# Optimization experiments

Measured on AMD Instinct MI355X. Metric: run time of the kernel, lower is better.

Reference implementation:

```python
import jax, jax.numpy as jnp
import numpy as np

B, T, D = 32, 2048, 512

def setup_inputs() -> dict:
    key = jax.random.key(0)
    k1, k2, k3 = jax.random.split(key, 3)
    return {
        "query": jax.random.normal(k1, (B, D), dtype=jnp.float32),
        "key": jax.random.normal(k2, (B, T, D), dtype=jnp.float32),
        "value": jax.random.normal(k3, (B, T, D), dtype=jnp.float32),
    }

def reference(query, key, value):
    # energy: [B, T] = bmm(key [B,T,D], query [B,D,1]).squeeze
    energy = jnp.einsum("btd,bd->bt", key, query)
    attention = jax.nn.softmax(energy, axis=1)  # over T, no scaling/masking (faithful)
    # context: [B, D] = bmm(attention [B,1,T], value [B,T,D]).squeeze
    out = jnp.einsum("bt,btd->bd", attention, value)
    return (out, attention)
```

## Files before the change

kernel.cpp:

```cpp
#include <hip/hip_runtime.h>

#define B_ 32
#define T_ 2048
#define D_ 512

__global__ __launch_bounds__(256) void energy_stats_kernel(
    const float* __restrict__ q,
    const float* __restrict__ key,
    float* __restrict__ energy,
    float* __restrict__ stats,
    float* __restrict__ out)
{
    const int b    = blockIdx.x >> 6;
    const int sub  = blockIdx.x & 63;
    const int wave = threadIdx.x >> 6;
    const int lane = threadIdx.x & 63;

    if (sub == 0 && threadIdx.x < 128) {
        const float4 z = {0.f, 0.f, 0.f, 0.f};
        ((float4*)out)[b * 128 + threadIdx.x] = z;
    }

    __shared__ float es[32];

    const float4 qv0 = ((const float4*)q)[b * 128 + lane];
    const float4 qv1 = ((const float4*)q)[b * 128 + 64 + lane];

    const int t0 = sub * 32 + wave * 8;
    const float4* kbase = (const float4*)key + ((size_t)b * T_ + t0) * 128;

#pragma unroll
    for (int r = 0; r < 8; ++r) {
        const float4 k0 = kbase[r * 128 + lane];
        const float4 k1 = kbase[r * 128 + 64 + lane];
        float acc = k0.x * qv0.x + k0.y * qv0.y + k0.z * qv0.z + k0.w * qv0.w
                  + k1.x * qv1.x + k1.y * qv1.y + k1.z * qv1.z + k1.w * qv1.w;
#pragma unroll
        for (int off = 32; off >= 1; off >>= 1)
            acc += __shfl_down(acc, off);
        if (lane == 0) {
            es[wave * 8 + r] = acc;
            energy[b * T_ + t0 + r] = acc;
        }
    }
    __syncthreads();

    if (threadIdx.x < 32) {
        const float e = es[threadIdx.x];
        float m = e;
#pragma unroll
        for (int off = 16; off >= 1; off >>= 1)
            m = fmaxf(m, __shfl_xor(m, off));
        float s = __expf(e - m);
#pragma unroll
        for (int off = 16; off >= 1; off >>= 1)
            s += __shfl_xor(s, off);
        if (threadIdx.x == 0) {
            stats[((size_t)b * 64 + sub) * 2 + 0] = m;
            stats[((size_t)b * 64 + sub) * 2 + 1] = s;
        }
    }
}

__global__ __launch_bounds__(256) void context_kernel(
    const float* __restrict__ energy,
    const float* __restrict__ stats,
    const float* __restrict__ value,
    float* __restrict__ attn,
    float* __restrict__ out)
{
    const int b   = blockIdx.x >> 6;
    const int sub = blockIdx.x & 63;
    const int t0  = sub * 32;
    const int tid = threadIdx.x;

    __shared__ float  MS[2];
    __shared__ float  attn_s[32];
    __shared__ float4 red4[128];

    if (tid < 64) {
        const float m_c = stats[((size_t)b * 64 + tid) * 2 + 0];
        const float s_c = stats[((size_t)b * 64 + tid) * 2 + 1];
        float M = m_c;
#pragma unroll
        for (int off = 32; off >= 1; off >>= 1)
            M = fmaxf(M, __shfl_xor(M, off));
        float S = s_c * __expf(m_c - M);
#pragma unroll
        for (int off = 32; off >= 1; off >>= 1)
            S += __shfl_xor(S, off);
        if (tid == 0) { MS[0] = M; MS[1] = S; }
    }
    __syncthreads();
    const float M    = MS[0];
    const float invS = 1.f / MS[1];

    if (tid < 32) {
        const float e = energy[b * T_ + t0 + tid];
        const float a = __expf(e - M) * invS;
        attn_s[tid] = a;
        attn[b * T_ + t0 + tid] = a;
    }
    __syncthreads();

    const int tg = tid >> 7;
    const int d4 = tid & 127;

    const float4* v4 = (const float4*)value + ((size_t)b * T_ + t0 + tg) * 128 + d4;
    float4 acc = {0.f, 0.f, 0.f, 0.f};
#pragma unroll
    for (int i = 0; i < 16; ++i) {
        const float a = attn_s[2 * i + tg];
        const float4 vv = v4[i * 256];
        acc.x += a * vv.x; acc.y += a * vv.y;
        acc.z += a * vv.z; acc.w += a * vv.w;
    }

    if (tg == 1) red4[d4] = acc;
    __syncthreads();
    if (tg == 0) {
        const float4 o = red4[d4];
        acc.x += o.x; acc.y += o.y; acc.z += o.z; acc.w += o.w;
        float* dst = out + (size_t)b * D_ + d4 * 4;
        atomicAdd(dst + 0, acc.x);
        atomicAdd(dst + 1, acc.y);
        atomicAdd(dst + 2, acc.z);
        atomicAdd(dst + 3, acc.w);
    }
}

extern "C" void kernel_launch(void* const* d_in, const int* in_sizes, int n_in,
                              void* d_out, int out_size, void* d_ws, size_t ws_size,
                              hipStream_t stream)
{
    const float* q     = (const float*)d_in[0];
    const float* key   = (const float*)d_in[1];
    const float* value = (const float*)d_in[2];

    float* out  = (float*)d_out;
    float* attn = out + B_ * D_;

    float* energy = (float*)d_ws;
    float* stats  = energy + B_ * T_;

    energy_stats_kernel<<<B_ * 64, 256, 0, stream>>>(q, key, energy, stats, out);
    context_kernel<<<B_ * 64, 256, 0, stream>>>(energy, stats, value, attn, out);
}
```

Baseline: 284.5 us.

## Fuse energy and context kernels with per-batch spin barrier and partial-sum reduction

Merges the two kernels into a single launch. Each of the 1024 blocks handles 64 timesteps, keeps its energies in shared memory, publishes its local softmax stats, and spin-waits on a per-batch counter until all 32 blocks of that batch have arrived. Output atomics are replaced by per-block partial sums, which the last-arriving block reduces. This removes the energy round-trip through global memory, a launch, and the float atomics. In exchange it relies on all blocks of a batch being co-resident, uses a bounded spin that could silently yield wrong results, and adds a memset launch.

```diff
diff --git a/kernel.cpp b/kernel.cpp
--- a/kernel.cpp
+++ b/kernel.cpp
@@ -4,90 +4,88 @@
 #define T_ 2048
 #define D_ 512
 
-__global__ __launch_bounds__(256) void energy_stats_kernel(
+__global__ __launch_bounds__(256) void fused_attn_kernel(
     const float* __restrict__ q,
     const float* __restrict__ key,
-    float* __restrict__ energy,
+    const float* __restrict__ value,
+    float* __restrict__ out,
+    float* __restrict__ attn,
+    int*   __restrict__ cnt,
     float* __restrict__ stats,
-    float* __restrict__ out)
+    float* __restrict__ partial)
 {
-    const int b    = blockIdx.x >> 6;
-    const int sub  = blockIdx.x & 63;
-    const int wave = threadIdx.x >> 6;
-    const int lane = threadIdx.x & 63;
+    const int b    = blockIdx.x >> 5;
+    const int sub  = blockIdx.x & 31;
+    const int t0   = sub * 64;
+    const int tid  = threadIdx.x;
+    const int wave = tid >> 6;
+    const int lane = tid & 63;
 
-    if (sub == 0 && threadIdx.x < 128) {
-        const float4 z = {0.f, 0.f, 0.f, 0.f};
-        ((float4*)out)[b * 128 + threadIdx.x] = z;
-    }
+    __shared__ float  es[64];
+    __shared__ float  asx[64];
+    __shared__ float  MS[2];
+    __shared__ float4 red4[128];
+    __shared__ int    isLast;
 
-    __shared__ float es[32];
-
-    const float4 qv0 = ((const float4*)q)[b * 128 + lane];
-    const float4 qv1 = ((const float4*)q)[b * 128 + 64 + lane];
-
-    const int t0 = sub * 32 + wave * 8;
-    const float4* kbase = (const float4*)key + ((size_t)b * T_ + t0) * 128;
-
+    {
+        const float4 qv0 = ((const float4*)q)[b * 128 + lane];
+        const float4 qv1 = ((const float4*)q)[b * 128 + 64 + lane];
+        const int tr = t0 + wave * 16;
+        const float4* kbase = (const float4*)key + ((size_t)b * T_ + tr) * 128;
+#pragma unroll 4
+        for (int r = 0; r < 16; ++r) {
+            const float4 k0 = kbase[r * 128 + lane];
+            const float4 k1 = kbase[r * 128 + 64 + lane];
+            float acc = k0.x * qv0.x + k0.y * qv0.y + k0.z * qv0.z + k0.w * qv0.w
+                      + k1.x * qv1.x + k1.y * qv1.y + k1.z * qv1.z + k1.w * qv1.w;
 #pragma unroll
-    for (int r = 0; r < 8; ++r) {
-        const float4 k0 = kbase[r * 128 + lane];
-        const float4 k1 = kbase[r * 128 + 64 + lane];
-        float acc = k0.x * qv0.x + k0.y * qv0.y + k0.z * qv0.z + k0.w * qv0.w
-                  + k1.x * qv1.x + k1.y * qv1.y + k1.z * qv1.z + k1.w * qv1.w;
-#pragma unroll
-        for (int off = 32; off >= 1; off >>= 1)
-            acc += __shfl_down(acc, off);
-        if (lane == 0) {
-            es[wave * 8 + r] = acc;
-            energy[b * T_ + t0 + r] = acc;
+            for (int off = 32; off >= 1; off >>= 1)
+                acc += __shfl_down(acc, off);
+            if (lane == 0)
+                es[wave * 16 + r] = acc;
         }
     }
     __syncthreads();
 
-    if (threadIdx.x < 32) {
-        const float e = es[threadIdx.x];
+    if (tid < 64) {
+        const float e = es[tid];
         float m = e;
 #pragma unroll
-        for (int off = 16; off >= 1; off >>= 1)
+        for (int off = 32; off >= 1; off >>= 1)
             m = fmaxf(m, __shfl_xor(m, off));
         float s = __expf(e - m);
 #pragma unroll
-        for (int off = 16; off >= 1; off >>= 1)
+        for (int off = 32; off >= 1; off >>= 1)
             s += __shfl_xor(s, off);
-        if (threadIdx.x == 0) {
-            stats[((size_t)b * 64 + sub) * 2 + 0] = m;
-            stats[((size_t)b * 64 + sub) * 2 + 1] = s;
+        if (tid == 0) {
+            stats[((size_t)b * 32 + sub) * 2 + 0] = m;
+            stats[((size_t)b * 32 + sub) * 2 + 1] = s;
+            __threadfence();
+            atomicAdd(&cnt[b], 1);
         }
     }
-}
 
-__global__ __launch_bounds__(256) void context_kernel(
-    const float* __restrict__ energy,
-    const float* __restrict__ stats,
-    const float* __restrict__ value,
-    float* __restrict__ attn,
-    float* __restrict__ out)
-{
-    const int b   = blockIdx.x >> 6;
-    const int sub = blockIdx.x & 63;
-    const int t0  = sub * 32;
-    const int tid = threadIdx.x;
+    if (tid == 0) {
+        int it = 0;
+        while (__hip_atomic_load(&cnt[b], __ATOMIC_ACQUIRE,
+                                 __HIP_MEMORY_SCOPE_AGENT) < 32) {
+            __builtin_amdgcn_s_sleep(2);
+            if (++it > (1 << 20)) break;
+        }
+        __threadfence();
+    }
+    __syncthreads();
 
-    __shared__ float  MS[2];
-    __shared__ float  attn_s[32];
-    __shared__ float4 red4[128];
-
-    if (tid < 64) {
-        const float m_c = stats[((size_t)b * 64 + tid) * 2 + 0];
-        const float s_c = stats[((size_t)b * 64 + tid) * 2 + 1];
+    if (tid < 32) {
+        const float m_c = stats[((size_t)b * 32 + tid) * 2 + 0];
+        const float s_c = stats[((size_t)b * 32 + tid) * 2 + 1];
         float M = m_c;
 #pragma unroll
-        for (int off = 32; off >= 1; off >>= 1)
+        for (int off = 16; off >= 1; off >>= 1)
             M = fmaxf(M, __shfl_xor(M, off));
         float S = s_c * __expf(m_c - M);
 #pragma unroll
-        for (int off = 32; off >= 1; off >>= 1)
+        for (int off = 16; off >= 1; off >>= 1)
             S += __shfl_xor(S, off);
         if (tid == 0) { MS[0] = M; MS[1] = S; }
     }
@@ -95,37 +93,51 @@
     const float M    = MS[0];
     const float invS = 1.f / MS[1];
 
-    if (tid < 32) {
-        const float e = energy[b * T_ + t0 + tid];
-        const float a = __expf(e - M) * invS;
-        attn_s[tid] = a;
+    if (tid < 64) {
+        const float a = __expf(es[tid] - M) * invS;
+        asx[tid] = a;
         attn[b * T_ + t0 + tid] = a;
     }
     __syncthreads();
 
     const int tg = tid >> 7;
     const int d4 = tid & 127;
-
-    const float4* v4 = (const float4*)value + ((size_t)b * T_ + t0 + tg) * 128 + d4;
-    float4 acc = {0.f, 0.f, 0.f, 0.f};
-#pragma unroll
-    for (int i = 0; i < 16; ++i) {
-        const float a = attn_s[2 * i + tg];
-        const float4 vv = v4[i * 256];
-        acc.x += a * vv.x; acc.y += a * vv.y;
-        acc.z += a * vv.z; acc.w += a * vv.w;
+    {
+        const float4* v4 = (const float4*)value + ((size_t)b * T_ + t0 + tg) * 128 + d4;
+        float4 acc = {0.f, 0.f, 0.f, 0.f};
+#pragma unroll 8
+        for (int i = 0; i < 32; ++i) {
+            const float a = asx[2 * i + tg];
+            const float4 vv = v4[i * 256];
+            acc.x += a * vv.x; acc.y += a * vv.y;
+            acc.z += a * vv.z; acc.w += a * vv.w;
+        }
+        if (tg == 1) red4[d4] = acc;
+        __syncthreads();
+        if (tg == 0) {
+            const float4 o = red4[d4];
+            acc.x += o.x; acc.y += o.y; acc.z += o.z; acc.w += o.w;
+            ((float4*)partial)[((size_t)b * 32 + sub) * 128 + d4] = acc;
+        }
     }
 
-    if (tg == 1) red4[d4] = acc;
+    if (tid == 0) __threadfence();
     __syncthreads();
-    if (tg == 0) {
-        const float4 o = red4[d4];
-        acc.x += o.x; acc.y += o.y; acc.z += o.z; acc.w += o.w;
-        float* dst = out + (size_t)b * D_ + d4 * 4;
-        atomicAdd(dst + 0, acc.x);
-        atomicAdd(dst + 1, acc.y);
-        atomicAdd(dst + 2, acc.z);
-        atomicAdd(dst + 3, acc.w);
+    if (tid == 0) {
+        __threadfence();
+        const int old = atomicAdd(&cnt[B_ + b], 1);
+        isLast = (old == 31);
+        if (isLast) __threadfence();
+    }
+    __syncthreads();
+    if (isLast && tid < 128) {
+        float4 s = {0.f, 0.f, 0.f, 0.f};
+#pragma unroll
+        for (int c = 0; c < 32; ++c) {
+            const float4 p = ((const float4*)partial)[((size_t)b * 32 + c) * 128 + tid];
+            s.x += p.x; s.y += p.y; s.z += p.z; s.w += p.w;
+        }
+        ((float4*)out)[b * 128 + tid] = s;
     }
 }
 
@@ -140,9 +152,11 @@
     float* out  = (float*)d_out;
     float* attn = out + B_ * D_;
 
-    float* energy = (float*)d_ws;
-    float* stats  = energy + B_ * T_;
+    int*   cnt     = (int*)d_ws;
+    float* stats   = (float*)d_ws + 2 * B_;
+    float* partial = stats + B_ * 32 * 2;
 
-    energy_stats_kernel<<<B_ * 64, 256, 0, stream>>>(q, key, energy, stats, out);
-    context_kernel<<<B_ * 64, 256, 0, stream>>>(energy, stats, value, attn, out);
+    hipMemsetAsync(cnt, 0, 2 * B_ * sizeof(int), stream);
+    fused_attn_kernel<<<B_ * 32, 256, 0, stream>>>(
+        q, key, value, out, attn, cnt, stats, partial);
 }
```

Result: slower. 508.1 us (+78.6%).

## Fuse value reduction into chunk kernel with flash-style local softmax rescaling

Applied to the files above, without the earlier changes.

Each 32-row chunk block now computes energies, a local softmax (exp relative to the chunk max) and the value-weighted partial context in one kernel, writing per-chunk partial outputs instead of energies. A small finalize kernel rescales the partials and the local attention weights by exp(m_c-M)/S to produce the exact output, replacing the per-element atomicAdds and the separate zeroing of the output. This lets key and value reads overlap in one pass and removes atomic contention, at the cost of a partial buffer (B*64*D floats) written and read back, and a finalize stage with low parallelism (64 blocks).

```diff
diff --git a/kernel.cpp b/kernel.cpp
--- a/kernel.cpp
+++ b/kernel.cpp
@@ -4,79 +4,100 @@
 #define T_ 2048
 #define D_ 512
 
-__global__ __launch_bounds__(256) void energy_stats_kernel(
+__global__ __launch_bounds__(256) void chunk_kernel(
     const float* __restrict__ q,
     const float* __restrict__ key,
-    float* __restrict__ energy,
+    const float* __restrict__ value,
+    float* __restrict__ a_loc,
     float* __restrict__ stats,
-    float* __restrict__ out)
+    float* __restrict__ partial)
 {
     const int b    = blockIdx.x >> 6;
     const int sub  = blockIdx.x & 63;
-    const int wave = threadIdx.x >> 6;
-    const int lane = threadIdx.x & 63;
+    const int t0   = sub * 32;
+    const int tid  = threadIdx.x;
+    const int wave = tid >> 6;
+    const int lane = tid & 63;
 
-    if (sub == 0 && threadIdx.x < 128) {
-        const float4 z = {0.f, 0.f, 0.f, 0.f};
-        ((float4*)out)[b * 128 + threadIdx.x] = z;
-    }
+    __shared__ float  es[32];
+    __shared__ float  asx[32];
+    __shared__ float4 red4[128];
 
-    __shared__ float es[32];
-
-    const float4 qv0 = ((const float4*)q)[b * 128 + lane];
-    const float4 qv1 = ((const float4*)q)[b * 128 + 64 + lane];
-
-    const int t0 = sub * 32 + wave * 8;
-    const float4* kbase = (const float4*)key + ((size_t)b * T_ + t0) * 128;
-
+    {
+        const float4 qv0 = ((const float4*)q)[b * 128 + lane];
+        const float4 qv1 = ((const float4*)q)[b * 128 + 64 + lane];
+        const int tr = t0 + wave * 8;
+        const float4* kbase = (const float4*)key + ((size_t)b * T_ + tr) * 128;
 #pragma unroll
-    for (int r = 0; r < 8; ++r) {
-        const float4 k0 = kbase[r * 128 + lane];
-        const float4 k1 = kbase[r * 128 + 64 + lane];
-        float acc = k0.x * qv0.x + k0.y * qv0.y + k0.z * qv0.z + k0.w * qv0.w
-                  + k1.x * qv1.x + k1.y * qv1.y + k1.z * qv1.z + k1.w * qv1.w;
+        for (int r = 0; r < 8; ++r) {
+            const float4 k0 = kbase[r * 128 + lane];
+            const float4 k1 = kbase[r * 128 + 64 + lane];
+            float acc = k0.x * qv0.x + k0.y * qv0.y + k0.z * qv0.z + k0.w * qv0.w
+                      + k1.x * qv1.x + k1.y * qv1.y + k1.z * qv1.z + k1.w * qv1.w;
 #pragma unroll
-        for (int off = 32; off >= 1; off >>= 1)
-            acc += __shfl_down(acc, off);
-        if (lane == 0) {
-            es[wave * 8 + r] = acc;
-            energy[b * T_ + t0 + r] = acc;
+            for (int off = 32; off >= 1; off >>= 1)
+                acc += __shfl_down(acc, off);
+            if (lane == 0)
+                es[wave * 8 + r] = acc;
         }
     }
     __syncthreads();
 
-    if (threadIdx.x < 32) {
-        const float e = es[threadIdx.x];
+    if (tid < 32) {
+        const float e = es[tid];
         float m = e;
 #pragma unroll
         for (int off = 16; off >= 1; off >>= 1)
             m = fmaxf(m, __shfl_xor(m, off));
-        float s = __expf(e - m);
+        const float a = __expf(e - m);
+        float s = a;
 #pragma unroll
         for (int off = 16; off >= 1; off >>= 1)
             s += __shfl_xor(s, off);
-        if (threadIdx.x == 0) {
+        asx[tid] = a;
+        a_loc[b * T_ + t0 + tid] = a;
+        if (tid == 0) {
             stats[((size_t)b * 64 + sub) * 2 + 0] = m;
             stats[((size_t)b * 64 + sub) * 2 + 1] = s;
         }
     }
+    __syncthreads();
+
+    const int tg = tid >> 7;
+    const int d4 = tid & 127;
+    const float4* v4 = (const float4*)value + ((size_t)b * T_ + t0 + tg) * 128 + d4;
+    float4 acc = {0.f, 0.f, 0.f, 0.f};
+#pragma unroll
+    for (int i = 0; i < 16; ++i) {
+        const float a = asx[2 * i + tg];
+        const float4 vv = v4[i * 256];
+        acc.x += a * vv.x; acc.y += a * vv.y;
+        acc.z += a * vv.z; acc.w += a * vv.w;
+    }
+    if (tg == 1) red4[d4] = acc;
+    __syncthreads();
+    if (tg == 0) {
+        const float4 o = red4[d4];
+        acc.x += o.x; acc.y += o.y; acc.z += o.z; acc.w += o.w;
+        ((float4*)partial)[((size_t)b * 64 + sub) * 128 + d4] = acc;
+    }
 }
 
-__global__ __launch_bounds__(256) void context_kernel(
-    const float* __restrict__ energy,
+__global__ __launch_bounds__(256) void finalize_kernel(
+    const float* __restrict__ a_loc,
     const float* __restrict__ stats,
-    const float* __restrict__ value,
-    float* __restrict__ attn,
-    float* __restrict__ out)
+    const float* __restrict__ partial,
+    float* __restrict__ out,
+    float* __restrict__ attn)
 {
-    const int b   = blockIdx.x >> 6;
-    const int sub = blockIdx.x & 63;
-    const int t0  = sub * 32;
-    const int tid = threadIdx.x;
+    const int b    = blockIdx.x >> 1;
+    const int h    = blockIdx.x & 1;
+    const int tid  = threadIdx.x;
+    const int lane = tid & 63;
+    const int qd   = tid >> 6;
 
-    __shared__ float  MS[2];
-    __shared__ float  attn_s[32];
-    __shared__ float4 red4[128];
+    __shared__ float  wc[64];
+    __shared__ float4 redo[256];
 
     if (tid < 64) {
         const float m_c = stats[((size_t)b * 64 + tid) * 2 + 0];
@@ -89,43 +110,41 @@
 #pragma unroll
         for (int off = 32; off >= 1; off >>= 1)
             S += __shfl_xor(S, off);
-        if (tid == 0) { MS[0] = M; MS[1] = S; }
-    }
-    __syncthreads();
-    const float M    = MS[0];
-    const float invS = 1.f / MS[1];
-
-    if (tid < 32) {
-        const float e = energy[b * T_ + t0 + tid];
-        const float a = __expf(e - M) * invS;
-        attn_s[tid] = a;
-        attn[b * T_ + t0 + tid] = a;
+        wc[tid] = __expf(m_c - M) / S;
     }
     __syncthreads();
 
-    const int tg = tid >> 7;
-    const int d4 = tid & 127;
-
-    const float4* v4 = (const float4*)value + ((size_t)b * T_ + t0 + tg) * 128 + d4;
-    float4 acc = {0.f, 0.f, 0.f, 0.f};
-#pragma unroll
-    for (int i = 0; i < 16; ++i) {
-        const float a = attn_s[2 * i + tg];
-        const float4 vv = v4[i * 256];
-        acc.x += a * vv.x; acc.y += a * vv.y;
-        acc.z += a * vv.z; acc.w += a * vv.w;
+    {
+        const int t = h * 1024 + tid * 4;
+        const float w = wc[t >> 5];
+        float4 a = ((const float4*)(a_loc + (size_t)b * T_))[h * 256 + tid];
+        a.x *= w; a.y *= w; a.z *= w; a.w *= w;
+        ((float4*)(attn + (size_t)b * T_))[h * 256 + tid] = a;
     }
 
-    if (tg == 1) red4[d4] = acc;
-    __syncthreads();
-    if (tg == 0) {
-        const float4 o = red4[d4];
-        acc.x += o.x; acc.y += o.y; acc.z += o.z; acc.w += o.w;
-        float* dst = out + (size_t)b * D_ + d4 * 4;
-        atomicAdd(dst + 0, acc.x);
-        atomicAdd(dst + 1, acc.y);
-        atomicAdd(dst + 2, acc.z);
-        atomicAdd(dst + 3, acc.w);
+    {
+        const int d4 = h * 64 + lane;
+        float4 acc = {0.f, 0.f, 0.f, 0.f};
+#pragma unroll
+        for (int i = 0; i < 16; ++i) {
+            const int c = qd * 16 + i;
+            const float w = wc[c];
+            const float4 p = ((const float4*)partial)[((size_t)b * 64 + c) * 128 + d4];
+            acc.x += w * p.x; acc.y += w * p.y;
+            acc.z += w * p.z; acc.w += w * p.w;
+        }
+        redo[tid] = acc;
+        __syncthreads();
+        if (qd == 0) {
+            const float4 a1 = redo[64 + lane];
+            const float4 a2 = redo[128 + lane];
+            const float4 a3 = redo[192 + lane];
+            acc.x += a1.x + a2.x + a3.x;
+            acc.y += a1.y + a2.y + a3.y;
+            acc.z += a1.z + a2.z + a3.z;
+            acc.w += a1.w + a2.w + a3.w;
+            ((float4*)out)[b * 128 + d4] = acc;
+        }
     }
 }
 
@@ -140,9 +159,10 @@
     float* out  = (float*)d_out;
     float* attn = out + B_ * D_;
 
-    float* energy = (float*)d_ws;
-    float* stats  = energy + B_ * T_;
+    float* a_loc   = (float*)d_ws;
+    float* stats   = a_loc + (size_t)B_ * T_;
+    float* partial = stats + (size_t)B_ * 64 * 2;
 
-    energy_stats_kernel<<<B_ * 64, 256, 0, stream>>>(q, key, energy, stats, out);
-    context_kernel<<<B_ * 64, 256, 0, stream>>>(energy, stats, value, attn, out);
+    chunk_kernel<<<B_ * 64, 256, 0, stream>>>(q, key, value, a_loc, stats, partial);
+    finalize_kernel<<<B_ * 2, 256, 0, stream>>>(a_loc, stats, partial, out, attn);
 }
```

After: 284.8 us. About the same (+0.1%).
